# Performance work log

Hardware: AMD Instinct MI355X
Metric: run time of the kernel (lower is better)

## Reference

```python
import jax, jax.numpy as jnp
import numpy as np

B, S, HID = 2, 2048, 2048
H, KVH, D = 16, 8, 128           # query heads, kv heads, head_dim
G = H // KVH                      # num_key_value_groups
EPS = 1e-6
SCALE = D ** -0.5
ROPE_THETA = 1e6


def _rope_tables():
    inv_freq = 1.0 / (ROPE_THETA ** (jnp.arange(0, D, 2, dtype=jnp.float32) / D))
    freqs = jnp.arange(S, dtype=jnp.float32)[:, None] * inv_freq[None, :]   # [S, D/2]
    emb = jnp.concatenate([freqs, freqs], axis=-1)                          # [S, D]
    cos = jnp.broadcast_to(jnp.cos(emb)[None], (B, S, D))
    sin = jnp.broadcast_to(jnp.sin(emb)[None], (B, S, D))
    return cos, sin


def setup_inputs() -> dict:
    key = jax.random.key(0)
    ks = jax.random.split(key, 6)
    hidden_states = jax.random.normal(ks[0], (B, S, HID), jnp.float32)
    cos, sin = _rope_tables()
    w = 0.02
    Wq = jax.random.normal(ks[1], (HID, H * D * 2), jnp.float32) * w  # gated: q + gate
    Wk = jax.random.normal(ks[2], (HID, KVH * D), jnp.float32) * w
    Wv = jax.random.normal(ks[3], (HID, KVH * D), jnp.float32) * w
    Wo = jax.random.normal(ks[4], (H * D, HID), jnp.float32) * w
    q_norm_w = jnp.ones((D,), jnp.float32)
    k_norm_w = jnp.ones((D,), jnp.float32)
    return {"hidden_states": hidden_states, "cos": cos, "sin": sin,
            "Wq": Wq, "Wk": Wk, "Wv": Wv, "Wo": Wo,
            "q_norm_w": q_norm_w, "k_norm_w": k_norm_w}


def _rms_norm(x, w):
    # per-head RMSNorm over last dim (head_dim), computed in fp32
    var = jnp.mean(jnp.square(x.astype(jnp.float32)), axis=-1, keepdims=True)
    return (x * jax.lax.rsqrt(var + EPS)) * w


def _rotate_half(x):
    x1, x2 = x[..., : D // 2], x[..., D // 2:]
    return jnp.concatenate([-x2, x1], axis=-1)


def reference(hidden_states, cos, sin, Wq, Wk, Wv, Wo, q_norm_w, k_norm_w):
    # q_proj with output gate
    mixed_q = hidden_states @ Wq                         # [B,S,H*2D]
    mixed_q = mixed_q.reshape(B, S, H, 2 * D)
    q, gate = mixed_q[..., :D], mixed_q[..., D:]          # [B,S,H,D] each
    gate = gate.reshape(B, S, H * D)
    k = (hidden_states @ Wk).reshape(B, S, KVH, D)
    v = (hidden_states @ Wv).reshape(B, S, KVH, D)

    # per-head QK RMSNorm, then to [B, heads, S, D]
    q = _rms_norm(q, q_norm_w).transpose(0, 2, 1, 3)      # [B,H,S,D]
    k = _rms_norm(k, k_norm_w).transpose(0, 2, 1, 3)      # [B,KVH,S,D]
    v = v.transpose(0, 2, 1, 3)                           # [B,KVH,S,D]

    # RoPE (cos/sin broadcast over head dim)
    c, s = cos[:, None], sin[:, None]                     # [B,1,S,D]
    q = q * c + _rotate_half(q) * s
    k = k * c + _rotate_half(k) * s

    # GQA causal attention without materializing repeated K/V
    qg = q.reshape(B, KVH, G, S, D)
    scores = jnp.einsum('bkgqd,bkld->bkgql', qg, k) * SCALE   # [B,KVH,G,S,S]
    causal = jnp.tril(jnp.ones((S, S), dtype=bool))
    scores = jnp.where(causal, scores, jnp.finfo(scores.dtype).min)
    probs = jax.nn.softmax(scores, axis=-1)
    out = jnp.einsum('bkgql,bkld->bkgqd', probs, v)           # [B,KVH,G,S,D]
    out = out.reshape(B, H, S, D).transpose(0, 2, 1, 3).reshape(B, S, H * D)

    # sigmoid-gated output, then o_proj
    out = out * jax.nn.sigmoid(gate)
    return out @ Wo
```

## Files before the change

kernel.cpp:

```cpp
#include <hip/hip_runtime.h>
#include <hip/hip_bf16.h>

#define B_ 2
#define S_ 2048
#define HID_ 2048
#define H_ 16
#define KVH_ 8
#define D_ 128
#define G_ 2
#define EPS_ 1e-6f
#define SCALE_ 0.08838834764831845f
#define SCALE2_ 0.1275313760443445f
#define NQKV 6144

typedef __hip_bfloat16 bf16;
typedef __attribute__((ext_vector_type(8))) short s8v;
typedef __attribute__((ext_vector_type(4))) float f4v;

__device__ __forceinline__ unsigned short f2b(float f) {
    __hip_bfloat16 h = __float2bfloat16(f);
    return *reinterpret_cast<unsigned short*>(&h);
}
__device__ __forceinline__ float b2f(short u) {
    unsigned int x = ((unsigned int)(unsigned short)u) << 16;
    return __builtin_bit_cast(float, x);
}

__device__ __forceinline__ f4v MFMA(s8v a, s8v b, f4v c) {
    return __builtin_amdgcn_mfma_f32_16x16x32_bf16(a, b, c, 0, 0, 0);
}

__device__ __forceinline__ void gl_lds16(const void* g, void* l) {
    __builtin_amdgcn_global_load_lds(
        (const __attribute__((address_space(1))) void*)g,
        (__attribute__((address_space(3))) void*)l, 16, 0, 0);
}

__device__ __forceinline__ void cstore(float* p, float v) { *p = v; }
__device__ __forceinline__ void cstore(short* p, float v) { *p = (short)f2b(v); }

template <int CTRL>
__device__ __forceinline__ float dpp_f(float x) {
    return __builtin_bit_cast(float,
        __builtin_amdgcn_update_dpp(0, __builtin_bit_cast(int, x), CTRL, 0xF, 0xF, true));
}
__device__ __forceinline__ float red16_max(float v) {
    v = fmaxf(v, dpp_f<0xB1>(v));
    v = fmaxf(v, dpp_f<0x4E>(v));
    v = fmaxf(v, dpp_f<0x124>(v));
    v = fmaxf(v, dpp_f<0x128>(v));
    return v;
}
__device__ __forceinline__ float red16_sum(float v) {
    v += dpp_f<0xB1>(v);
    v += dpp_f<0x4E>(v);
    v += dpp_f<0x124>(v);
    v += dpp_f<0x128>(v);
    return v;
}

__global__ __launch_bounds__(256) void f2bf_kernel(const float* __restrict__ in,
                                                   short* __restrict__ out, int n4) {
    int i = blockIdx.x * 256 + threadIdx.x;
    if (i >= n4) return;
    const float4 v = *(const float4*)(in + (size_t)i * 4);
    ushort4 o;
    o.x = f2b(v.x); o.y = f2b(v.y); o.z = f2b(v.z); o.w = f2b(v.w);
    *(ushort4*)(out + (size_t)i * 4) = o;
}

__global__ __launch_bounds__(256) void transpose_conv(const float* __restrict__ in,
                                                      short* __restrict__ out,
                                                      int K, int N) {
    __shared__ short t[32][33];
    const int n0 = blockIdx.x * 32, k0 = blockIdx.y * 32;
    const int tx = threadIdx.x, ty = threadIdx.y;
#pragma unroll
    for (int j = 0; j < 4; j++) {
        const int r = ty + j * 8;
        t[r][tx] = (short)f2b(in[(size_t)(k0 + r) * N + n0 + tx]);
    }
    __syncthreads();
#pragma unroll
    for (int j = 0; j < 4; j++) {
        const int r = ty + j * 8;
        out[(size_t)(n0 + r) * K + k0 + tx] = t[tx][r];
    }
}

__global__ __launch_bounds__(256) void transpose_v(const short* __restrict__ in,
                                                   short* __restrict__ out) {
    __shared__ short t[32][33];
    const int s0 = blockIdx.x * 32, d0 = blockIdx.y * 32, bk = blockIdx.z;
    const int b = bk / KVH_, kvh = bk % KVH_;
    const short* ip = in + (size_t)b * S_ * NQKV + kvh * D_;
    const int tx = threadIdx.x, ty = threadIdx.y;
#pragma unroll
    for (int j = 0; j < 4; j++) {
        const int r = ty + j * 8;
        t[r][tx] = ip[(size_t)(s0 + r) * NQKV + d0 + tx];
    }
    __syncthreads();
#pragma unroll
    for (int j = 0; j < 4; j++) {
        const int r = ty + j * 8;
        out[((size_t)bk * D_ + d0 + r) * S_ + s0 + tx] = t[tx][r];
    }
}

__global__ __launch_bounds__(512, 2) void gemm256(const short* __restrict__ A,
                                                  const short* __restrict__ Bt,
                                                  short* __restrict__ C,
                                                  int M, int N, int K) {
    __shared__ __align__(16) short As[3][256][32];
    __shared__ __align__(16) short Bs[3][256][32];
    const int tid = threadIdx.x;
    const int w = tid >> 6, l = tid & 63;
    const int lr = l & 15, g = l >> 4;
    const int nwg = gridDim.x * gridDim.y;
    int bid = blockIdx.y * gridDim.x + blockIdx.x;
    bid = (bid & 7) * (nwg >> 3) + (bid >> 3);
    const int bx = bid % gridDim.x, by = bid / gridDim.x;
    const int row0 = by * 256, col0 = bx * 256;
    const int wr = w >> 2, wc = w & 3;

    f4v acc[8][4];
#pragma unroll
    for (int i = 0; i < 8; i++)
#pragma unroll
        for (int j = 0; j < 4; j++) acc[i][j] = (f4v)0.f;

    const int srow = l >> 2;
    const int schunk = (l & 3) ^ ((l >> 3) & 3);
    const int rdslot = (g ^ ((lr >> 1) & 3)) * 8;

    auto stageA = [&](int buf, int t) {
        const int kt = t * 32;
#pragma unroll
        for (int i = 0; i < 2; i++) {
            const int rb = w * 32 + i * 16;
            gl_lds16(A + (size_t)(row0 + rb + srow) * K + kt + schunk * 8,
                     &As[buf][rb][0]);
        }
    };
    auto stageB = [&](int buf, int t) {
        const int kt = t * 32;
#pragma unroll
        for (int i = 0; i < 2; i++) {
            const int rb = w * 32 + i * 16;
            gl_lds16(Bt + (size_t)(col0 + rb + srow) * K + kt + schunk * 8,
                     &Bs[buf][rb][0]);
        }
    };

    const int nt = K >> 5;
    stageA(0, 0); stageB(0, 0);
    stageA(1, 1); stageB(1, 1);

#pragma unroll 1
    for (int t = 0; t < nt; t++) {
        const int buf = t % 3;
        const int nbuf = (t + 2) % 3;

        __builtin_amdgcn_sched_barrier(0);
        if (t + 1 < nt) {
            asm volatile("s_waitcnt vmcnt(4)" ::: "memory");
        } else {
            asm volatile("s_waitcnt vmcnt(0)" ::: "memory");
        }
        __builtin_amdgcn_sched_barrier(0);
        __builtin_amdgcn_s_barrier();
        __builtin_amdgcn_sched_barrier(0);

        s8v b[4], a[4];
#pragma unroll
        for (int ni = 0; ni < 4; ni++)
            b[ni] = *(const s8v*)&Bs[buf][wc * 64 + ni * 16 + lr][rdslot];
#pragma unroll
        for (int mi = 0; mi < 4; mi++)
            a[mi] = *(const s8v*)&As[buf][wr * 128 + mi * 16 + lr][rdslot];
        if (t + 2 < nt) stageA(nbuf, t + 2);
        __builtin_amdgcn_s_setprio(1);
#pragma unroll
        for (int mi = 0; mi < 4; mi++)
#pragma unroll
            for (int ni = 0; ni < 4; ni++)
                acc[mi][ni] = MFMA(a[mi], b[ni], acc[mi][ni]);
        __builtin_amdgcn_s_setprio(0);
        __builtin_amdgcn_s_barrier();
        __builtin_amdgcn_sched_barrier(0);

        s8v a2[4];
#pragma unroll
        for (int mi = 0; mi < 4; mi++)
            a2[mi] = *(const s8v*)&As[buf][wr * 128 + (4 + mi) * 16 + lr][rdslot];
        if (t + 2 < nt) stageB(nbuf, t + 2);
        __builtin_amdgcn_s_setprio(1);
#pragma unroll
        for (int mi = 0; mi < 4; mi++)
#pragma unroll
            for (int ni = 0; ni < 4; ni++)
                acc[4 + mi][ni] = MFMA(a2[mi], b[ni], acc[4 + mi][ni]);
        __builtin_amdgcn_s_setprio(0);
    }

#pragma unroll
    for (int mi = 0; mi < 8; mi++)
#pragma unroll
        for (int ni = 0; ni < 4; ni++) {
            const int row = row0 + wr * 128 + mi * 16 + g * 4;
            const int col = col0 + wc * 64 + ni * 16 + lr;
#pragma unroll
            for (int j = 0; j < 4; j++)
                cstore(&C[(size_t)(row + j) * N + col], acc[mi][ni][j]);
        }
}

template <typename CT, int GATED>
__global__ __launch_bounds__(256) void gemm_bt(const short* __restrict__ A,
                                               const short* __restrict__ Bt,
                                               CT* __restrict__ C,
                                               int M, int N, int K) {
    __shared__ __align__(16) short As[2][128][32];
    __shared__ __align__(16) short Bs[2][128][32];
    const int tid = threadIdx.x;
    const int w = tid >> 6, l = tid & 63;
    const int lr = l & 15, g = l >> 4;
    const int nwg = gridDim.x * gridDim.y;
    int bid = blockIdx.y * gridDim.x + blockIdx.x;
    bid = (bid & 7) * (nwg >> 3) + (bid >> 3);
    const int bx = bid % gridDim.x, by = bid / gridDim.x;
    const int row0 = by * 128, col0 = bx * 128;
    const int wr = w >> 1, wc = w & 1;

    f4v acc[4][4];
#pragma unroll
    for (int i = 0; i < 4; i++)
#pragma unroll
        for (int j = 0; j < 4; j++) acc[i][j] = (f4v)0.f;

    const int srow = l >> 2;
    const int sg = (l & 3) ^ ((srow >> 1) & 3);

    auto stage = [&](int buf, int kt) {
        const int k = kt + sg * 8;
#pragma unroll
        for (int i = 0; i < 2; i++) {
            const int rb = (w * 2 + i) * 16;
            size_t aoff;
            if constexpr (GATED)
                aoff = (size_t)(row0 + rb + srow) * NQKV + ((k >> 7) << 8) + (k & 127);
            else
                aoff = (size_t)(row0 + rb + srow) * K + k;
            gl_lds16(A + aoff, &As[buf][rb][0]);
            gl_lds16(Bt + (size_t)(col0 + rb + srow) * K + k, &Bs[buf][rb][0]);
        }
    };

    const int nt = K >> 5;
    stage(0, 0);
    stage(1, 32);
    const int rdslot = (g ^ ((lr >> 1) & 3)) * 8;

#pragma unroll 1
    for (int t = 0; t < nt; t++) {
        const int cur = t & 1;
        if (t + 1 < nt) {
            asm volatile("s_waitcnt vmcnt(4)" ::: "memory");
        } else {
            asm volatile("s_waitcnt vmcnt(0)" ::: "memory");
        }
        __builtin_amdgcn_s_barrier();
        __builtin_amdgcn_sched_barrier(0);

        s8v a[4], b[4];
#pragma unroll
        for (int mi = 0; mi < 4; mi++)
            a[mi] = *(const s8v*)&As[cur][wr * 64 + mi * 16 + lr][rdslot];
#pragma unroll
        for (int ni = 0; ni < 4; ni++)
            b[ni] = *(const s8v*)&Bs[cur][wc * 64 + ni * 16 + lr][rdslot];

        asm volatile("s_waitcnt lgkmcnt(0)" ::: "memory");
        __builtin_amdgcn_sched_barrier(0);
        __builtin_amdgcn_s_barrier();
        __builtin_amdgcn_sched_barrier(0);

        if (t + 2 < nt) stage(cur, (t + 2) * 32);

#pragma unroll
        for (int mi = 0; mi < 4; mi++)
#pragma unroll
            for (int ni = 0; ni < 4; ni++)
                acc[mi][ni] = MFMA(a[mi], b[ni], acc[mi][ni]);
    }

#pragma unroll
    for (int mi = 0; mi < 4; mi++)
#pragma unroll
        for (int ni = 0; ni < 4; ni++) {
            const int row = row0 + wr * 64 + mi * 16 + g * 4;
            const int col = col0 + wc * 64 + ni * 16 + lr;
#pragma unroll
            for (int j = 0; j < 4; j++)
                cstore(&C[(size_t)(row + j) * N + col], acc[mi][ni][j]);
        }
}

__global__ __launch_bounds__(128) void norm_rope(const bf16* __restrict__ src,
                                                 const float* __restrict__ normw,
                                                 const float* __restrict__ cosb,
                                                 const float* __restrict__ sinb,
                                                 bf16* __restrict__ dst,
                                                 int NH, int rowStride, int chanStride) {
    const int idx = blockIdx.x;
    const int h = idx % NH;
    const int s = (idx / NH) % S_;
    const int b = idx / (NH * S_);
    const int d = threadIdx.x;

    const size_t src_i = (size_t)(b * S_ + s) * rowStride + h * chanStride + d;
    const size_t dst_i = (((size_t)b * NH + h) * S_ + s) * D_ + d;

    float x = __bfloat162float(src[src_i]);
    float sq = x * x;
#pragma unroll
    for (int o = 32; o > 0; o >>= 1) sq += __shfl_down(sq, o);
    __shared__ float red[2];
    __shared__ float sh[128];
    if ((d & 63) == 0) red[d >> 6] = sq;
    __syncthreads();
    const float var = (red[0] + red[1]) * (1.f / 128.f);
    const float xn = x * rsqrtf(var + EPS_) * normw[d];
    sh[d] = xn;
    __syncthreads();
    const float rot = (d < 64) ? -sh[d + 64] : sh[d - 64];
    const size_t cs_i = ((size_t)b * S_ + s) * D_ + d;
    dst[dst_i] = __float2bfloat16(xn * cosb[cs_i] + rot * sinb[cs_i]);
}

__global__ __launch_bounds__(256, 1) void flash_mfma(const short* __restrict__ qro,
                                                     const short* __restrict__ kro,
                                                     const short* __restrict__ vt,
                                                     short* __restrict__ qkv) {
    __shared__ __align__(16) short Ks[2][64][128];
    __shared__ __align__(16) short Vs[2][128][64];
    __shared__ __align__(16) short Pl[4][32][84];

    const int tid = threadIdx.x;
    const int w = tid >> 6, l = tid & 63;
    const int lr = l & 15, g = l >> 4;
    const int bx = blockIdx.x;
    const int bh = blockIdx.y;
    const int b = bh >> 4, h = bh & 15;
    const int kvh = h >> 1;

    const short* qbase = qro + (size_t)(b * H_ + h) * S_ * D_;
    const short* kbase = kro + (size_t)(b * KVH_ + kvh) * S_ * D_;
    const short* vbase = vt + (size_t)(b * KVH_ + kvh) * D_ * S_;

    auto stage = [&](int buf, int kt) {
        const int kb0 = kt * 64;
#pragma unroll
        for (int i = 0; i < 4; i++) {
            const int li = w * 4 + i;
            {
                const int r = li * 4 + (l >> 4);
                const int sgk = (l & 15) ^ (r & 7);
                gl_lds16(kbase + (size_t)(kb0 + r) * D_ + sgk * 8, &Ks[buf][li * 4][0]);
            }
            {
                const int r = li * 8 + (l >> 3);
                const int sgv = (l & 7) ^ (r & 7);
                gl_lds16(vbase + (size_t)r * S_ + kb0 + sgv * 8, &Vs[buf][li * 8][0]);
            }
        }
    };

#pragma unroll 1
    for (int seg = 0; seg < 2; seg++) {
        const int qt = seg ? bx : (15 - bx);
        const int q0 = qt * 128;
        const int qw0 = q0 + w * 32;

        if (seg) __syncthreads();

        s8v qa[2][4];
#pragma unroll
        for (int mi = 0; mi < 2; mi++)
#pragma unroll
            for (int kc = 0; kc < 4; kc++)
                qa[mi][kc] = *(const s8v*)(qbase + (size_t)(qw0 + mi * 16 + lr) * D_ +
                                           kc * 32 + g * 8);

        f4v oacc[2][8];
#pragma unroll
        for (int mi = 0; mi < 2; mi++)
#pragma unroll
            for (int i = 0; i < 8; i++) oacc[mi][i] = (f4v)0.f;
        float m[2][4], lsum[2][4];
#pragma unroll
        for (int mi = 0; mi < 2; mi++)
#pragma unroll
            for (int j = 0; j < 4; j++) { m[mi][j] = -3e38f; lsum[mi][j] = 0.f; }

        const int nkt = 2 * (qt + 1);
        stage(0, 0);
        int cur = 0;
        for (int kt = 0; kt < nkt; kt++) {
            __syncthreads();
            if (kt + 1 < nkt) stage(cur ^ 1, kt + 1);
            const int kb0 = kt * 64;

            f4v sacc[2][4];
#pragma unroll
            for (int mi = 0; mi < 2; mi++)
#pragma unroll
                for (int ni = 0; ni < 4; ni++) sacc[mi][ni] = (f4v)0.f;
            __builtin_amdgcn_s_setprio(1);
#pragma unroll
            for (int ni = 0; ni < 4; ni++) {
                const int r = ni * 16 + lr;
#pragma unroll
                for (int kc = 0; kc < 4; kc++) {
                    const int ph = (kc * 4 + g) ^ (r & 7);
                    const s8v kb = *(const s8v*)&Ks[cur][r][ph * 8];
                    sacc[0][ni] = MFMA(qa[0][kc], kb, sacc[0][ni]);
                    sacc[1][ni] = MFMA(qa[1][kc], kb, sacc[1][ni]);
                }
            }
            __builtin_amdgcn_s_setprio(0);

            const bool masked = (kt >= nkt - 2);
            float p[2][4][4], tmax[2][4];
#pragma unroll
            for (int mi = 0; mi < 2; mi++)
#pragma unroll
                for (int j = 0; j < 4; j++) {
                    float v0 = -3e38f;
#pragma unroll
                    for (int ni = 0; ni < 4; ni++) {
                        float sc = sacc[mi][ni][j] * SCALE2_;
                        if (masked && (kb0 + ni * 16 + lr > qw0 + mi * 16 + g * 4 + j))
                            sc = -3e38f;
                        p[mi][ni][j] = sc;
                        v0 = fmaxf(v0, sc);
                    }
                    tmax[mi][j] = v0;
                }
#pragma unroll
            for (int mi = 0; mi < 2; mi++)
#pragma unroll
                for (int j = 0; j < 4; j++) tmax[mi][j] = red16_max(tmax[mi][j]);

            bool needb = false;
#pragma unroll
            for (int mi = 0; mi < 2; mi++)
#pragma unroll
                for (int j = 0; j < 4; j++)
                    needb = needb || (tmax[mi][j] > m[mi][j] + 7.f);
            const bool doresc = __any((int)needb);

            float cj[2][4], psum[2][4];
#pragma unroll
            for (int mi = 0; mi < 2; mi++)
#pragma unroll
                for (int j = 0; j < 4; j++) {
                    float mn = m[mi][j];
                    if (doresc) {
                        mn = fmaxf(m[mi][j], tmax[mi][j]);
                        cj[mi][j] = __builtin_amdgcn_exp2f(m[mi][j] - mn);
                        m[mi][j] = mn;
                    }
                    float ps = 0.f;
#pragma unroll
                    for (int ni = 0; ni < 4; ni++) {
                        const float e = __builtin_amdgcn_exp2f(p[mi][ni][j] - mn);
                        p[mi][ni][j] = e;
                        ps += e;
                    }
                    psum[mi][j] = ps;
                }

#pragma unroll
            for (int mi = 0; mi < 2; mi++)
#pragma unroll
                for (int ni = 0; ni < 4; ni++)
#pragma unroll
                    for (int j = 0; j < 4; j++)
                        Pl[w][mi * 16 + g * 4 + j][ni * 16 + lr] =
                            (short)f2b(p[mi][ni][j]);

#pragma unroll
            for (int mi = 0; mi < 2; mi++)
#pragma unroll
                for (int j = 0; j < 4; j++) psum[mi][j] = red16_sum(psum[mi][j]);

            if (doresc) {
#pragma unroll
                for (int mi = 0; mi < 2; mi++) {
#pragma unroll
                    for (int j = 0; j < 4; j++)
                        lsum[mi][j] = lsum[mi][j] * cj[mi][j] + psum[mi][j];
#pragma unroll
                    for (int di = 0; di < 8; di++)
#pragma unroll
                        for (int j = 0; j < 4; j++) oacc[mi][di][j] *= cj[mi][j];
                }
            } else {
#pragma unroll
                for (int mi = 0; mi < 2; mi++)
#pragma unroll
                    for (int j = 0; j < 4; j++) lsum[mi][j] += psum[mi][j];
            }

            __builtin_amdgcn_s_setprio(1);
#pragma unroll
            for (int kk = 0; kk < 2; kk++) {
                const s8v pa0 = *(const s8v*)&Pl[w][lr][kk * 32 + g * 8];
                const s8v pa1 = *(const s8v*)&Pl[w][16 + lr][kk * 32 + g * 8];
#pragma unroll
                for (int di = 0; di < 8; di++) {
                    const int r = di * 16 + lr;
                    const int ph = (kk * 4 + g) ^ (r & 7);
                    const s8v vb = *(const s8v*)&Vs[cur][r][ph * 8];
                    oacc[0][di] = MFMA(pa0, vb, oacc[0][di]);
                    oacc[1][di] = MFMA(pa1, vb, oacc[1][di]);
                }
            }
            __builtin_amdgcn_s_setprio(0);
            cur ^= 1;
        }

        float linv[2][4];
#pragma unroll
        for (int mi = 0; mi < 2; mi++)
#pragma unroll
            for (int j = 0; j < 4; j++) linv[mi][j] = 1.f / lsum[mi][j];
#pragma unroll
        for (int mi = 0; mi < 2; mi++)
#pragma unroll
            for (int di = 0; di < 8; di++) {
                const int d = di * 16 + lr;
#pragma unroll
                for (int j = 0; j < 4; j++) {
                    const int q = qw0 + mi * 16 + g * 4 + j;
                    const size_t base = (size_t)(b * S_ + q) * NQKV + h * 256;
                    const float gate = b2f(qkv[base + 128 + d]);
                    const float o = oacc[mi][di][j] * linv[mi][j] *
                                    (1.f / (1.f + __expf(-gate)));
                    qkv[base + d] = (short)f2b(o);
                }
            }
    }
}

extern "C" void kernel_launch(void* const* d_in, const int* in_sizes, int n_in,
                              void* d_out, int out_size, void* d_ws, size_t ws_size,
                              hipStream_t stream) {
    const float* hs = (const float*)d_in[0];
    const float* cosb = (const float*)d_in[1];
    const float* sinb = (const float*)d_in[2];
    const float* Wq = (const float*)d_in[3];
    const float* Wk = (const float*)d_in[4];
    const float* Wv = (const float*)d_in[5];
    const float* Wo = (const float*)d_in[6];
    const float* qnw = (const float*)d_in[7];
    const float* knw = (const float*)d_in[8];
    float* out = (float*)d_out;

    short* ws = (short*)d_ws;
    short* Wot = ws;
    short* Wt  = ws + 4194304;
    short* hsb = ws + 16777216;
    short* qkv = ws + 25165824;
    short* qro = Wt;
    short* kro = Wt + 8388608;
    short* vtb = hsb;

    const int M = B_ * S_;
    const dim3 t32x8(32, 8, 1);

    f2bf_kernel<<<8192, 256, 0, stream>>>(hs, hsb, 2097152);
    transpose_conv<<<dim3(128, 64), t32x8, 0, stream>>>(Wq, Wt, HID_, 4096);
    transpose_conv<<<dim3(32, 64), t32x8, 0, stream>>>(Wk, Wt + (size_t)4096 * 2048, HID_, 1024);
    transpose_conv<<<dim3(32, 64), t32x8, 0, stream>>>(Wv, Wt + (size_t)5120 * 2048, HID_, 1024);
    transpose_conv<<<dim3(64, 64), t32x8, 0, stream>>>(Wo, Wot, 2048, 2048);

    gemm256<<<dim3(24, 16), 512, 0, stream>>>(hsb, Wt, qkv, M, NQKV, HID_);

    norm_rope<<<dim3(B_ * S_ * H_), 128, 0, stream>>>((const bf16*)qkv, qnw, cosb, sinb,
                                                      (bf16*)qro, H_, NQKV, 256);
    norm_rope<<<dim3(B_ * S_ * KVH_), 128, 0, stream>>>((const bf16*)(qkv + 4096), knw, cosb, sinb,
                                                        (bf16*)kro, KVH_, NQKV, 128);

    transpose_v<<<dim3(64, 4, 16), t32x8, 0, stream>>>(qkv + 5120, vtb);

    flash_mfma<<<dim3(8, 32), 256, 0, stream>>>(qro, kro, vtb, qkv);

    gemm_bt<float, 1><<<dim3(16, 32), 256, 0, stream>>>(qkv, Wot, out, M, HID_, 2048);
}
```

Before: 361.2 us.

## Single-buffer K/V in flash kernel for two blocks per CU; fold scale into Q

Drops the LDS double buffer for K and V in the flash attention kernel and raises launch bounds to allow two blocks per CU. Loads are now issued synchronously at the start of each tile, with a barrier after the PV step. The softmax scale (including log2e) is moved into the Q norm/rope kernel, so the per-score multiply goes away. This trades in-block prefetch overlap for cross-block occupancy overlap, and it may raise register pressure or lose latency hiding. Scaling Q before the bf16 rounding also changes rounding slightly.

```diff
diff --git a/kernel.cpp b/kernel.cpp
--- a/kernel.cpp
+++ b/kernel.cpp
@@ -312,7 +312,8 @@
                                                  const float* __restrict__ cosb,
                                                  const float* __restrict__ sinb,
                                                  bf16* __restrict__ dst,
-                                                 int NH, int rowStride, int chanStride) {
+                                                 int NH, int rowStride, int chanStride,
+                                                 float oscale) {
     const int idx = blockIdx.x;
     const int h = idx % NH;
     const int s = (idx / NH) % S_;
@@ -336,15 +337,15 @@
     __syncthreads();
     const float rot = (d < 64) ? -sh[d + 64] : sh[d - 64];
     const size_t cs_i = ((size_t)b * S_ + s) * D_ + d;
-    dst[dst_i] = __float2bfloat16(xn * cosb[cs_i] + rot * sinb[cs_i]);
-}
-
-__global__ __launch_bounds__(256, 1) void flash_mfma(const short* __restrict__ qro,
+    dst[dst_i] = __float2bfloat16((xn * cosb[cs_i] + rot * sinb[cs_i]) * oscale);
+}
+
+__global__ __launch_bounds__(256, 2) void flash_mfma(const short* __restrict__ qro,
                                                      const short* __restrict__ kro,
                                                      const short* __restrict__ vt,
                                                      short* __restrict__ qkv) {
-    __shared__ __align__(16) short Ks[2][64][128];
-    __shared__ __align__(16) short Vs[2][128][64];
+    __shared__ __align__(16) short Ks[64][128];
+    __shared__ __align__(16) short Vs[128][64];
     __shared__ __align__(16) short Pl[4][32][84];
 
     const int tid = threadIdx.x;
@@ -359,7 +360,7 @@
     const short* kbase = kro + (size_t)(b * KVH_ + kvh) * S_ * D_;
     const short* vbase = vt + (size_t)(b * KVH_ + kvh) * D_ * S_;
 
-    auto stage = [&](int buf, int kt) {
+    auto stage = [&](int kt) {
         const int kb0 = kt * 64;
 #pragma unroll
         for (int i = 0; i < 4; i++) {
@@ -367,12 +368,12 @@
             {
                 const int r = li * 4 + (l >> 4);
                 const int sgk = (l & 15) ^ (r & 7);
-                gl_lds16(kbase + (size_t)(kb0 + r) * D_ + sgk * 8, &Ks[buf][li * 4][0]);
+                gl_lds16(kbase + (size_t)(kb0 + r) * D_ + sgk * 8, &Ks[li * 4][0]);
             }
             {
                 const int r = li * 8 + (l >> 3);
                 const int sgv = (l & 7) ^ (r & 7);
-                gl_lds16(vbase + (size_t)r * S_ + kb0 + sgv * 8, &Vs[buf][li * 8][0]);
+                gl_lds16(vbase + (size_t)r * S_ + kb0 + sgv * 8, &Vs[li * 8][0]);
             }
         }
     };
@@ -383,8 +384,6 @@
         const int q0 = qt * 128;
         const int qw0 = q0 + w * 32;
 
-        if (seg) __syncthreads();
-
         s8v qa[2][4];
 #pragma unroll
         for (int mi = 0; mi < 2; mi++)
@@ -405,11 +404,9 @@
             for (int j = 0; j < 4; j++) { m[mi][j] = -3e38f; lsum[mi][j] = 0.f; }
 
         const int nkt = 2 * (qt + 1);
-        stage(0, 0);
-        int cur = 0;
         for (int kt = 0; kt < nkt; kt++) {
+            stage(kt);
             __syncthreads();
-            if (kt + 1 < nkt) stage(cur ^ 1, kt + 1);
             const int kb0 = kt * 64;
 
             f4v sacc[2][4];
@@ -424,7 +421,7 @@
 #pragma unroll
                 for (int kc = 0; kc < 4; kc++) {
                     const int ph = (kc * 4 + g) ^ (r & 7);
-                    const s8v kb = *(const s8v*)&Ks[cur][r][ph * 8];
+                    const s8v kb = *(const s8v*)&Ks[r][ph * 8];
                     sacc[0][ni] = MFMA(qa[0][kc], kb, sacc[0][ni]);
                     sacc[1][ni] = MFMA(qa[1][kc], kb, sacc[1][ni]);
                 }
@@ -440,7 +437,7 @@
                     float v0 = -3e38f;
 #pragma unroll
                     for (int ni = 0; ni < 4; ni++) {
-                        float sc = sacc[mi][ni][j] * SCALE2_;
+                        float sc = sacc[mi][ni][j];
                         if (masked && (kb0 + ni * 16 + lr > qw0 + mi * 16 + g * 4 + j))
                             sc = -3e38f;
                         p[mi][ni][j] = sc;
@@ -523,13 +520,13 @@
                 for (int di = 0; di < 8; di++) {
                     const int r = di * 16 + lr;
                     const int ph = (kk * 4 + g) ^ (r & 7);
-                    const s8v vb = *(const s8v*)&Vs[cur][r][ph * 8];
+                    const s8v vb = *(const s8v*)&Vs[r][ph * 8];
                     oacc[0][di] = MFMA(pa0, vb, oacc[0][di]);
                     oacc[1][di] = MFMA(pa1, vb, oacc[1][di]);
                 }
             }
             __builtin_amdgcn_s_setprio(0);
-            cur ^= 1;
+            __syncthreads();
         }
 
         float linv[2][4];
@@ -590,9 +587,9 @@
     gemm256<<<dim3(24, 16), 512, 0, stream>>>(hsb, Wt, qkv, M, NQKV, HID_);
 
     norm_rope<<<dim3(B_ * S_ * H_), 128, 0, stream>>>((const bf16*)qkv, qnw, cosb, sinb,
-                                                      (bf16*)qro, H_, NQKV, 256);
+                                                      (bf16*)qro, H_, NQKV, 256, SCALE2_);
     norm_rope<<<dim3(B_ * S_ * KVH_), 128, 0, stream>>>((const bf16*)(qkv + 4096), knw, cosb, sinb,
-                                                        (bf16*)kro, KVH_, NQKV, 128);
+                                                        (bf16*)kro, KVH_, NQKV, 128, 1.f);
 
     transpose_v<<<dim3(64, 4, 16), t32x8, 0, stream>>>(qkv + 5120, vtb);
 
```

Result: no change. 356.2 us (-1.4%).
